# Optimization experiments

Hardware: AMD Instinct MI355X
Metric: run time of the kernel (lower is better)

Reference implementation:

```python
import jax, jax.numpy as jnp
import numpy as np

EMBED_DIM = 1024
NUM_HEADS = 16
HEAD_DIM = EMBED_DIM // NUM_HEADS
SCALING = HEAD_DIM ** (-0.5)
BSZ, SEQ = 2, 2048


def setup_inputs() -> dict:
    key = jax.random.key(0)
    ks = jax.random.split(key, 12)
    s = 1.0 / np.sqrt(EMBED_DIM)
    query = jax.random.normal(ks[0], (BSZ, SEQ, EMBED_DIM), dtype=jnp.float32)
    return {
        "query": query,
        "key": query,
        "value": query,
        "attn_bias": jax.random.normal(ks[1], (BSZ, NUM_HEADS, SEQ, SEQ), dtype=jnp.float32) * 0.1,
        "Wq": jax.random.normal(ks[2], (EMBED_DIM, EMBED_DIM), dtype=jnp.float32) * s,
        "bq": jax.random.normal(ks[3], (EMBED_DIM,), dtype=jnp.float32) * 0.01,
        "Wk": jax.random.normal(ks[4], (EMBED_DIM, EMBED_DIM), dtype=jnp.float32) * s,
        "bk": jax.random.normal(ks[5], (EMBED_DIM,), dtype=jnp.float32) * 0.01,
        "Wv": jax.random.normal(ks[6], (EMBED_DIM, EMBED_DIM), dtype=jnp.float32) * s,
        "bv": jax.random.normal(ks[7], (EMBED_DIM,), dtype=jnp.float32) * 0.01,
        "Wo": jax.random.normal(ks[8], (EMBED_DIM, EMBED_DIM), dtype=jnp.float32) * s,
        "bo": jax.random.normal(ks[9], (EMBED_DIM,), dtype=jnp.float32) * 0.01,
    }


def reference(query, key, value, attn_bias, Wq, bq, Wk, bk, Wv, bv, Wo, bo):
    # Self-attention: k and v are computed from `query` (key/value args ignored
    # by the original module). torch Linear: y = x @ W.T + b
    B, T, E = query.shape
    H, D = NUM_HEADS, HEAD_DIM
    q = (query @ Wq.T + bq) * SCALING
    k = query @ Wk.T + bk
    v = query @ Wv.T + bv
    # [B, T, H, D]
    q = q.reshape(B, T, H, D)
    k = k.reshape(B, T, H, D)
    v = v.reshape(B, T, H, D)
    # scores: [B, H, T, T]
    scores = jnp.einsum("bthd,bshd->bhts", q, k) + attn_bias
    probs = jax.nn.softmax(scores, axis=-1)
    # attention output: [B, T, H, D] -> [B, T, E]
    attn = jnp.einsum("bhts,bshd->bthd", probs, v).reshape(B, T, E)
    out = attn @ Wo.T + bo
    # need_weights=True default: average attention weights over heads [B, T, T]
    avg_weights = probs.mean(axis=1)
    return out, avg_weights
```

## Files before the change

kernel.cpp:

```cpp
#include <hip/hip_runtime.h>
#include <hip/hip_bf16.h>

#define B_ 2
#define H_ 16
#define T_ 2048
#define D_ 64
#define ED_ 1024

typedef __attribute__((ext_vector_type(8))) short bf16x8;
typedef __attribute__((ext_vector_type(4))) short bf16x4;
typedef __attribute__((ext_vector_type(4))) float f32x4;

__device__ __forceinline__ void gload16(const void* g, void* l) {
  __builtin_amdgcn_global_load_lds(
      (const __attribute__((address_space(1))) unsigned int*)(uintptr_t)g,
      (__attribute__((address_space(3))) unsigned int*)(uintptr_t)l,
      16, 0, 0);
}

__device__ __forceinline__ short f2b(float v) {
  return __builtin_bit_cast(short, __float2bfloat16(v));
}

__global__ __launch_bounds__(256) void convert_f32_bf16(
    const float* __restrict__ x, const float* __restrict__ wq, const float* __restrict__ wk,
    const float* __restrict__ wv, const float* __restrict__ wo,
    __hip_bfloat16* __restrict__ xb, __hip_bfloat16* __restrict__ wqb,
    __hip_bfloat16* __restrict__ wkb, __hip_bfloat16* __restrict__ wvb,
    __hip_bfloat16* __restrict__ wob)
{
  int id = blockIdx.x * 256 + threadIdx.x;
  size_t e0 = (size_t)id * 4;
  const float* src; __hip_bfloat16* dst; size_t off;
  if (e0 < 4194304) { src = x; dst = xb; off = e0; }
  else {
    size_t r = e0 - 4194304;
    int wsel = (int)(r >> 20);
    off = r & 1048575;
    src = (wsel == 0) ? wq : (wsel == 1) ? wk : (wsel == 2) ? wv : wo;
    dst = (wsel == 0) ? wqb : (wsel == 1) ? wkb : (wsel == 2) ? wvb : wob;
  }
  float4 v = *(const float4*)(src + off);
  __hip_bfloat16 o[4];
  o[0] = __float2bfloat16(v.x); o[1] = __float2bfloat16(v.y);
  o[2] = __float2bfloat16(v.z); o[3] = __float2bfloat16(v.w);
  *(ushort4*)(dst + off) = *(ushort4*)o;
}

struct GemmP {
  const __hip_bfloat16* A;
  const __hip_bfloat16* Bw[3];
  const float* bias[3];
  void* out[3];
  float scale[3];
  int mode[3];
};

__global__ __launch_bounds__(256, 2) void gemm_nt(GemmP p)
{
  __shared__ __hip_bfloat16 As[128 * 64];
  __shared__ __hip_bfloat16 Bs[128 * 64];
  const int tid = threadIdx.x;
  const int z = blockIdx.z;
  const __hip_bfloat16* A = p.A;
  const __hip_bfloat16* Bw = p.Bw[z];
  const int bm0 = blockIdx.x * 128, bn0 = blockIdx.y * 128;
  const int l = tid & 63, w = tid >> 6;
  const int wr = w >> 1, wc = w & 1;
  const int lhi = l >> 4, llo = l & 15;
  const int swl = (llo & 7) << 3;

  f32x4 acc[4][4];
#pragma unroll
  for (int m = 0; m < 4; ++m)
#pragma unroll
    for (int n = 0; n < 4; ++n) acc[m][n] = (f32x4){0.f, 0.f, 0.f, 0.f};

  for (int kt = 0; kt < 1024; kt += 64) {
#pragma unroll
    for (int j = 0; j < 4; ++j) {
      int off = j * 2048 + tid * 8;
      int row = off >> 6;
      int col = off & 63;
      int cs = col ^ ((row & 7) << 3);
      gload16(&A[(size_t)(bm0 + row) * 1024 + kt + cs], &As[off]);
      gload16(&Bw[(size_t)(bn0 + row) * 1024 + kt + cs], &Bs[off]);
    }
    __syncthreads();
#pragma unroll
    for (int kk = 0; kk < 2; ++kk) {
      bf16x8 af[4], bf[4];
#pragma unroll
      for (int m = 0; m < 4; ++m)
        af[m] = *(const bf16x8*)&As[(wr * 64 + m * 16 + llo) * 64 + ((kk * 32 + lhi * 8) ^ swl)];
#pragma unroll
      for (int n = 0; n < 4; ++n)
        bf[n] = *(const bf16x8*)&Bs[(wc * 64 + n * 16 + llo) * 64 + ((kk * 32 + lhi * 8) ^ swl)];
#pragma unroll
      for (int m = 0; m < 4; ++m)
#pragma unroll
        for (int n = 0; n < 4; ++n)
          acc[m][n] = __builtin_amdgcn_mfma_f32_16x16x32_bf16(af[m], bf[n], acc[m][n], 0, 0, 0);
    }
    __syncthreads();
  }

  const float* bias = p.bias[z];
  const float scale = p.scale[z];
  const int mode = p.mode[z];
  float bv[4];
#pragma unroll
  for (int n = 0; n < 4; ++n) bv[n] = bias[bn0 + wc * 64 + n * 16 + llo];
#pragma unroll
  for (int m = 0; m < 4; ++m) {
    int rowb = bm0 + wr * 64 + m * 16 + lhi * 4;
#pragma unroll
    for (int n = 0; n < 4; ++n) {
      int col = bn0 + wc * 64 + n * 16 + llo;
#pragma unroll
      for (int r = 0; r < 4; ++r) {
        float v = (acc[m][n][r] + bv[n]) * scale;
        int row = rowb + r;
        if (mode == 0) {
          ((__hip_bfloat16*)p.out[z])[(size_t)row * 1024 + col] = __float2bfloat16(v);
        } else if (mode == 1) {
          ((float*)p.out[z])[(size_t)row * 1024 + col] = v;
        } else {
          int bb = row >> 11, t = row & 2047;
          int hh = col >> 6, d = col & 63;
          ((__hip_bfloat16*)p.out[z])[((size_t)((bb * 16 + hh) * 64 + d)) * 2048 + t] =
              __float2bfloat16(v);
        }
      }
    }
  }
}

__global__ __launch_bounds__(256, 4) void attn_fwd(
    const __hip_bfloat16* __restrict__ qb,
    const __hip_bfloat16* __restrict__ kb,
    const __hip_bfloat16* __restrict__ vT,
    const float* __restrict__ bias,
    unsigned char* __restrict__ Ebuf,
    float* __restrict__ invl,
    __hip_bfloat16* __restrict__ attn)
{
  __shared__ __hip_bfloat16 Ks[2][64 * 64];
  __shared__ __hip_bfloat16 Vs[2][64 * 64];
  __shared__ __hip_bfloat16 Ps[64 * 64];
  const int tid = threadIdx.x;
  const int l = tid & 63, w = tid >> 6;
  const int lhi = l >> 4, llo = l & 15;
  const int swl = (llo & 7) << 3;
  const int qt = blockIdx.x, h = blockIdx.y, b = blockIdx.z;
  const int t0 = qt * 64;
  const int tl = w * 16 + llo;
  const __hip_bfloat16* kbase = kb + ((size_t)b * 2048) * 1024 + h * 64;
  const __hip_bfloat16* vbase = vT + ((size_t)((b * 16 + h) * 64)) * 2048;
  const float* brow = bias + (((size_t)(b * 16 + h)) * 2048 + t0 + tl) * 2048;
  unsigned char* erow = Ebuf + (((size_t)(b * 16 + h)) * 2048 + t0 + tl) * 2048;

  bf16x8 qa[2];
#pragma unroll
  for (int kk = 0; kk < 2; ++kk)
    qa[kk] = *(const bf16x8*)&qb[((size_t)(b * 2048 + t0 + tl)) * 1024 +
                                 h * 64 + kk * 32 + lhi * 8];

  f32x4 acc_o[4];
#pragma unroll
  for (int f = 0; f < 4; ++f) acc_o[f] = (f32x4){0.f, 0.f, 0.f, 0.f};
  float lrun = 0.f;

#define STAGE(BUF, S0)                                                         \
  do {                                                                         \
    _Pragma("unroll") for (int j = 0; j < 2; ++j) {                            \
      int off = j * 2048 + tid * 8;                                            \
      int row = off >> 6, col = off & 63;                                      \
      int cs = col ^ ((row & 7) << 3);                                         \
      gload16(&kbase[(size_t)((S0) + row) * 1024 + cs], &Ks[BUF][off]);        \
      gload16(&vbase[(size_t)row * 2048 + (S0) + cs], &Vs[BUF][off]);          \
    }                                                                          \
  } while (0)

#define BLOAD(DST, S0)                                                         \
  do {                                                                         \
    _Pragma("unroll") for (int f = 0; f < 4; ++f)                              \
        DST[f] = *(const f32x4*)&brow[(S0) + f * 16 + lhi * 4];                \
  } while (0)

  f32x4 bA[4], bB[4];
  STAGE(0, 0);
  BLOAD(bA, 0);
  __syncthreads();

#define BODY(CUR, BC, BN, IT)                                                  \
  do {                                                                         \
    const int s0 = (IT) * 64;                                                  \
    if ((IT) < 31) {                                                           \
      STAGE(CUR ^ 1, s0 + 64);                                                 \
      BLOAD(BN, s0 + 64);                                                      \
    }                                                                          \
    f32x4 sa[4];                                                               \
    _Pragma("unroll") for (int f = 0; f < 4; ++f)                              \
        sa[f] = (f32x4){0.f, 0.f, 0.f, 0.f};                                   \
    _Pragma("unroll") for (int kk = 0; kk < 2; ++kk) {                         \
      _Pragma("unroll") for (int f = 0; f < 4; ++f) {                          \
        bf16x8 kf = *(const bf16x8*)&Ks[CUR][(f * 16 + llo) * 64 +             \
                                            ((kk * 32 + lhi * 8) ^ swl)];      \
        sa[f] = __builtin_amdgcn_mfma_f32_16x16x32_bf16(kf, qa[kk], sa[f],     \
                                                        0, 0, 0);              \
      }                                                                        \
    }                                                                          \
    float rsum = 0.f;                                                          \
    _Pragma("unroll") for (int f = 0; f < 4; ++f) {                            \
      float ev[4];                                                             \
      _Pragma("unroll") for (int r = 0; r < 4; ++r) {                          \
        ev[r] = __expf(sa[f][r] + BC[f][r]);                                   \
        rsum += ev[r];                                                         \
      }                                                                        \
      bf16x4 pw;                                                               \
      pw[0] = f2b(ev[0]); pw[1] = f2b(ev[1]);                                  \
      pw[2] = f2b(ev[2]); pw[3] = f2b(ev[3]);                                  \
      *(bf16x4*)&Ps[tl * 64 + ((f * 16 + lhi * 4) ^ swl)] = pw;                \
      int e01 = __builtin_amdgcn_cvt_pk_fp8_f32(ev[0] * 0.0625f,               \
                                                ev[1] * 0.0625f, 0, 0);        \
      int e = __builtin_amdgcn_cvt_pk_fp8_f32(ev[2] * 0.0625f,                 \
                                              ev[3] * 0.0625f, e01, 1);        \
      *(unsigned int*)&erow[s0 + f * 16 + lhi * 4] = (unsigned int)e;          \
    }                                                                          \
    rsum += __shfl_xor(rsum, 16);                                              \
    rsum += __shfl_xor(rsum, 32);                                              \
    lrun += rsum;                                                              \
    _Pragma("unroll") for (int kk = 0; kk < 2; ++kk) {                         \
      bf16x8 pa = *(const bf16x8*)&Ps[tl * 64 + ((kk * 32 + lhi * 8) ^ swl)];  \
      _Pragma("unroll") for (int f = 0; f < 4; ++f) {                          \
        bf16x8 vf = *(const bf16x8*)&Vs[CUR][(f * 16 + llo) * 64 +             \
                                            ((kk * 32 + lhi * 8) ^ swl)];      \
        acc_o[f] = __builtin_amdgcn_mfma_f32_16x16x32_bf16(pa, vf, acc_o[f],   \
                                                           0, 0, 0);           \
      }                                                                        \
    }                                                                          \
    __syncthreads();                                                           \
  } while (0)

  for (int i2 = 0; i2 < 16; ++i2) {
    BODY(0, bA, bB, 2 * i2);
    BODY(1, bB, bA, 2 * i2 + 1);
  }
#undef BODY
#undef BLOAD
#undef STAGE

  float invs = 1.f / lrun;
  float inv4[4];
#pragma unroll
  for (int r = 0; r < 4; ++r) inv4[r] = __shfl(invs, lhi * 4 + r);
#pragma unroll
  for (int f = 0; f < 4; ++f) {
    int d = f * 16 + llo;
#pragma unroll
    for (int r = 0; r < 4; ++r) {
      int t = t0 + w * 16 + lhi * 4 + r;
      attn[((size_t)(b * 2048 + t)) * 1024 + h * 64 + d] =
          __float2bfloat16(acc_o[f][r] * inv4[r]);
    }
  }
  if (l < 16)
    invl[((size_t)(b * 16 + h)) * 2048 + t0 + w * 16 + l] = invs;
}

__global__ __launch_bounds__(256) void avgw_k(
    const unsigned char* __restrict__ Ebuf, const float* __restrict__ invl,
    float* __restrict__ outw)
{
  int c = blockIdx.x * 256 + threadIdx.x;
  int b = c >> 18;
  int rem = c & 262143;
  int t = rem >> 7;
  int s0 = (rem & 127) << 4;
  float acc[16];
#pragma unroll
  for (int i = 0; i < 16; ++i) acc[i] = 0.f;
#pragma unroll
  for (int hh = 0; hh < 16; ++hh) {
    float inv = invl[((size_t)(b * 16 + hh)) * 2048 + t];
    uint4 evv = *(const uint4*)&Ebuf[(((size_t)(b * 16 + hh)) * 2048 + t) * 2048 + s0];
    unsigned int dw[4] = {evv.x, evv.y, evv.z, evv.w};
#pragma unroll
    for (int q = 0; q < 4; ++q) {
      acc[q * 4 + 0] += __builtin_amdgcn_cvt_f32_fp8(dw[q], 0) * inv;
      acc[q * 4 + 1] += __builtin_amdgcn_cvt_f32_fp8(dw[q], 1) * inv;
      acc[q * 4 + 2] += __builtin_amdgcn_cvt_f32_fp8(dw[q], 2) * inv;
      acc[q * 4 + 3] += __builtin_amdgcn_cvt_f32_fp8(dw[q], 3) * inv;
    }
  }
  float* o = outw + ((size_t)(b * 2048 + t)) * 2048 + s0;
#pragma unroll
  for (int q = 0; q < 4; ++q)
    *(float4*)(o + q * 4) = make_float4(acc[q * 4], acc[q * 4 + 1], acc[q * 4 + 2], acc[q * 4 + 3]);
}

extern "C" void kernel_launch(void* const* d_in, const int* in_sizes, int n_in,
                              void* d_out, int out_size, void* d_ws, size_t ws_size,
                              hipStream_t stream) {
  const float* query     = (const float*)d_in[0];
  const float* attn_bias = (const float*)d_in[3];
  const float* Wq = (const float*)d_in[4];
  const float* bq = (const float*)d_in[5];
  const float* Wk = (const float*)d_in[6];
  const float* bk = (const float*)d_in[7];
  const float* Wv = (const float*)d_in[8];
  const float* bv = (const float*)d_in[9];
  const float* Wo = (const float*)d_in[10];
  const float* bo = (const float*)d_in[11];
  float* out = (float*)d_out;

  char* ws = (char*)d_ws;
  __hip_bfloat16* xb   = (__hip_bfloat16*)(ws + 0);
  __hip_bfloat16* wqb  = (__hip_bfloat16*)(ws + 8388608);
  __hip_bfloat16* wkb  = (__hip_bfloat16*)(ws + 10485760);
  __hip_bfloat16* wvb  = (__hip_bfloat16*)(ws + 12582912);
  __hip_bfloat16* wob  = (__hip_bfloat16*)(ws + 14680064);
  __hip_bfloat16* qbf  = (__hip_bfloat16*)(ws + 16777216);
  __hip_bfloat16* kbf  = (__hip_bfloat16*)(ws + 25165824);
  __hip_bfloat16* vTb  = (__hip_bfloat16*)(ws + 33554432);
  __hip_bfloat16* atnb = (__hip_bfloat16*)(ws + 41943040);
  float*          linv = (float*)(ws + 50331648);
  unsigned char*  Ebuf = (unsigned char*)(ws + 50593792);

  convert_f32_bf16<<<8192, 256, 0, stream>>>(query, Wq, Wk, Wv, Wo, xb, wqb, wkb, wvb, wob);

  GemmP gp{};
  gp.A = xb;
  gp.Bw[0] = wqb; gp.Bw[1] = wkb; gp.Bw[2] = wvb;
  gp.bias[0] = bq; gp.bias[1] = bk; gp.bias[2] = bv;
  gp.out[0] = qbf; gp.out[1] = kbf; gp.out[2] = vTb;
  gp.scale[0] = 0.125f; gp.scale[1] = 1.f; gp.scale[2] = 1.f;
  gp.mode[0] = 0; gp.mode[1] = 0; gp.mode[2] = 2;
  gemm_nt<<<dim3(32, 8, 3), 256, 0, stream>>>(gp);

  attn_fwd<<<dim3(32, 16, 2), 256, 0, stream>>>(qbf, kbf, vTb, attn_bias, Ebuf, linv, atnb);

  avgw_k<<<2048, 256, 0, stream>>>(Ebuf, linv, out + 4194304);

  GemmP go{};
  go.A = atnb;
  go.Bw[0] = wob; go.bias[0] = bo; go.out[0] = out;
  go.scale[0] = 1.f; go.mode[0] = 1;
  gemm_nt<<<dim3(32, 8, 1), 256, 0, stream>>>(go);
}
```

Baseline: 320.4 us.

## Use partial vmcnt waits and raw barriers to overlap next-tile loads

Replaces __syncthreads in the attention loop with explicit s_waitcnt vmcnt(N) and s_barrier, so the prefetched K/V tile and bias loads for the next iteration can stay in flight while the current tile is consumed. It also changes the P write/read indexing and swizzle in LDS. The hand-tuned vmcnt counts depend on the exact number of outstanding loads per iteration, so any mismatch could produce a race or stale data. The Ps indexing change, which uses w and llo, may also change correctness if tl does not map the same way.

Result: no change. 320.4 us (+0.0%).

```diff
diff --git a/kernel.cpp b/kernel.cpp
--- a/kernel.cpp
+++ b/kernel.cpp
@@ -18,6 +18,10 @@
       16, 0, 0);
 }
 
+__device__ __forceinline__ float b2f(short s) {
+  unsigned int u = ((unsigned int)(unsigned short)s) << 16;
+  return __builtin_bit_cast(float, u);
+}
 __device__ __forceinline__ short f2b(float v) {
   return __builtin_bit_cast(short, __float2bfloat16(v));
 }
@@ -173,8 +177,8 @@
 
 #define STAGE(BUF, S0)                                                         \
   do {                                                                         \
-    _Pragma("unroll") for (int j = 0; j < 2; ++j) {                            \
-      int off = j * 2048 + tid * 8;                                            \
+    _Pragma("unroll") for (int j2 = 0; j2 < 2; ++j2) {                         \
+      int off = j2 * 2048 + tid * 8;                                           \
       int row = off >> 6, col = off & 63;                                      \
       int cs = col ^ ((row & 7) << 3);                                         \
       gload16(&kbase[(size_t)((S0) + row) * 1024 + cs], &Ks[BUF][off]);        \
@@ -189,9 +193,12 @@
   } while (0)
 
   f32x4 bA[4], bB[4];
+
   STAGE(0, 0);
   BLOAD(bA, 0);
-  __syncthreads();
+  asm volatile("s_waitcnt vmcnt(0)" ::: "memory");
+  __builtin_amdgcn_sched_barrier(0);
+  __builtin_amdgcn_s_barrier();
 
 #define BODY(CUR, BC, BN, IT)                                                  \
   do {                                                                         \
@@ -199,7 +206,14 @@
     if ((IT) < 31) {                                                           \
       STAGE(CUR ^ 1, s0 + 64);                                                 \
       BLOAD(BN, s0 + 64);                                                      \
-    }                                                                          \
+            \
+      asm volatile("s_waitcnt vmcnt(12)" ::: "memory");                        \
+    } else {                                                                   \
+      asm volatile("s_waitcnt vmcnt(4)" ::: "memory");                         \
+    }                                                                          \
+    __builtin_amdgcn_sched_barrier(0);                                         \
+    __builtin_amdgcn_s_barrier();                                              \
+          \
     f32x4 sa[4];                                                               \
     _Pragma("unroll") for (int f = 0; f < 4; ++f)                              \
         sa[f] = (f32x4){0.f, 0.f, 0.f, 0.f};                                   \
@@ -211,6 +225,7 @@
                                                         0, 0, 0);              \
       }                                                                        \
     }                                                                          \
+     \
     float rsum = 0.f;                                                          \
     _Pragma("unroll") for (int f = 0; f < 4; ++f) {                            \
       float ev[4];                                                             \
@@ -221,18 +236,21 @@
       bf16x4 pw;                                                               \
       pw[0] = f2b(ev[0]); pw[1] = f2b(ev[1]);                                  \
       pw[2] = f2b(ev[2]); pw[3] = f2b(ev[3]);                                  \
-      *(bf16x4*)&Ps[tl * 64 + ((f * 16 + lhi * 4) ^ swl)] = pw;                \
+      *(bf16x4*)&Ps[tl * 64 + ((f * 16 + lhi * 4) ^ ((llo & 7) << 3))] = pw;   \
       int e01 = __builtin_amdgcn_cvt_pk_fp8_f32(ev[0] * 0.0625f,               \
                                                 ev[1] * 0.0625f, 0, 0);        \
       int e = __builtin_amdgcn_cvt_pk_fp8_f32(ev[2] * 0.0625f,                 \
                                               ev[3] * 0.0625f, e01, 1);        \
       *(unsigned int*)&erow[s0 + f * 16 + lhi * 4] = (unsigned int)e;          \
     }                                                                          \
+                \
     rsum += __shfl_xor(rsum, 16);                                              \
     rsum += __shfl_xor(rsum, 32);                                              \
     lrun += rsum;                                                              \
+                                                       \
     _Pragma("unroll") for (int kk = 0; kk < 2; ++kk) {                         \
-      bf16x8 pa = *(const bf16x8*)&Ps[tl * 64 + ((kk * 32 + lhi * 8) ^ swl)];  \
+      bf16x8 pa = *(const bf16x8*)&Ps[(w * 16 + llo) * 64 +                    \
+                                      ((kk * 32 + lhi * 8) ^ swl)];            \
       _Pragma("unroll") for (int f = 0; f < 4; ++f) {                          \
         bf16x8 vf = *(const bf16x8*)&Vs[CUR][(f * 16 + llo) * 64 +             \
                                             ((kk * 32 + lhi * 8) ^ swl)];      \
@@ -240,7 +258,10 @@
                                                            0, 0, 0);           \
       }                                                                        \
     }                                                                          \
-    __syncthreads();                                                           \
+         \
+    asm volatile("s_waitcnt lgkmcnt(0)" ::: "memory");                         \
+    __builtin_amdgcn_sched_barrier(0);                                         \
+    __builtin_amdgcn_s_barrier();                                              \
   } while (0)
 
   for (int i2 = 0; i2 < 16; ++i2) {
```
